# Kernel tuning notes

Hardware: AMD Instinct MI355X
Metric: run time of the kernel (lower is better)

Reference implementation:

```python
import jax, jax.numpy as jnp
import numpy as np

NEG_BIG = -9e15
ALPHA = 0.2  # leakyrelu slope


def setup_inputs() -> dict:
    key = jax.random.key(0)
    k1, k2, k3, k4 = jax.random.split(key, 4)
    N, Fin, Fout = 8192, 256, 256
    input = jax.random.normal(k1, (N, Fin), dtype=jnp.float32)
    adj = jax.random.randint(k2, (N, N), 0, 2, dtype=jnp.int32)
    W = jax.random.normal(k3, (Fin, Fout), dtype=jnp.float32) * (1.0 / np.sqrt(Fin))
    a = jax.random.normal(k4, (2 * Fout, 1), dtype=jnp.float32) * (1.0 / np.sqrt(Fout))
    return {"input": input, "adj": adj, "W": W, "a": a}


def reference(input, adj, W, a):
    # h: [N, F]
    h = input @ W
    Fout = h.shape[1]
    # Fused score: e_ij = leakyrelu(h_i . a[:F] + h_j . a[F:])
    s1 = h @ a[:Fout, 0]   # [N]
    s2 = h @ a[Fout:, 0]   # [N]
    e = s1[:, None] + s2[None, :]            # [N, N]
    e = jnp.where(e >= 0, e, ALPHA * e)      # leaky relu
    e = jnp.where(adj > 0, e, NEG_BIG)       # mask
    attention = jax.nn.softmax(e, axis=1)    # row softmax
    h_prime = attention @ h                  # [N, F]
    return jax.nn.elu(h_prime)               # concat=True -> elu
```

## Files before the change

### kernel.cpp

```cpp
#include <hip/hip_runtime.h>
#include <hip/hip_bf16.h>

#define LRALPHA 0.2f
#define LOG2E 1.4426950408889634f

typedef __attribute__((ext_vector_type(8))) short frag_ab;
typedef __attribute__((ext_vector_type(4))) float frag_cd;
typedef int   iv4 __attribute__((ext_vector_type(4)));
typedef float fv4 __attribute__((ext_vector_type(4)));
typedef float fv2 __attribute__((ext_vector_type(2)));
typedef unsigned int uv4 __attribute__((ext_vector_type(4)));

static __device__ __forceinline__ unsigned short f2bf(float f) {
  __hip_bfloat16 b = __float2bfloat16(f);
  unsigned short u;
  __builtin_memcpy(&u, &b, 2);
  return u;
}

static __device__ __forceinline__ uv4 make_w(const iv4* ca, const fv4* cv,
                                             float c1, float c2, float& zloc) {
  uv4 out;
#pragma unroll
  for (int g = 0; g < 2; ++g) {
#pragma unroll
    for (int h = 0; h < 2; ++h) {
      unsigned b0, b1;
#pragma unroll
      for (int e = 0; e < 2; ++e) {
        const int idx = h * 2 + e;
        const float u = fmaf(cv[g][idx], LOG2E, c1);
        const float m = fmaxf(u, LRALPHA * u);
        float w = exp2f(m - c2);
        w = ca[g][idx] ? w : 0.f;
        const unsigned bb = __float_as_uint(w);
        zloc += __uint_as_float(bb & 0xFFFF0000u);
        if (e == 0) b0 = bb; else b1 = bb;
      }
      out[g * 2 + h] = __builtin_amdgcn_perm(b1, b0, 0x07060302u);
    }
  }
  return out;
}

__global__ __launch_bounds__(256, 4) void gat_hproj(
    const float* __restrict__ X, const float* __restrict__ W,
    const float* __restrict__ avec,
    float* __restrict__ s1, float* __restrict__ s2,
    unsigned* __restrict__ s2key,
    unsigned short* __restrict__ hT) {
  const int tid = threadIdx.x;
  const int row0 = blockIdx.x * 16;
  const float* Xb = X + (size_t)row0 * 256;
  const int c = tid;

  fv2 acc2[8];
#pragma unroll
  for (int p = 0; p < 8; ++p) acc2[p] = (fv2){0.f, 0.f};

  for (int k = 0; k < 256; k += 4) {
    float wq[4];
#pragma unroll
    for (int i = 0; i < 4; ++i) wq[i] = W[(k + i) * 256 + c];
#pragma unroll
    for (int p = 0; p < 8; ++p) {
      const float* xr0 = Xb + (2 * p) * 256 + k;
      const float* xr1 = Xb + (2 * p + 1) * 256 + k;
#pragma unroll
      for (int i = 0; i < 4; ++i) {
        const fv2 xv = {xr0[i], xr1[i]};
        const fv2 wv = {wq[i], wq[i]};
        acc2[p] += xv * wv;
      }
    }
  }

  alignas(16) unsigned short hu[16];
#pragma unroll
  for (int r = 0; r < 16; ++r) hu[r] = f2bf(acc2[r >> 1][r & 1]);
  uv4* hdst = (uv4*)(hT + (size_t)c * 8192 + row0);
  hdst[0] = *(const uv4*)&hu[0];
  hdst[1] = *(const uv4*)&hu[8];

  const float a1c = avec[c];
  const float a2c = avec[256 + c];
  const int lane = tid & 63, wave = tid >> 6;
  __shared__ float r1[4][16], r2[4][16];
#pragma unroll
  for (int r = 0; r < 16; ++r) {
    const float av = acc2[r >> 1][r & 1];
    float v1 = av * a1c;
    float v2 = av * a2c;
#pragma unroll
    for (int off = 32; off > 0; off >>= 1) {
      v1 += __shfl_down(v1, off);
      v2 += __shfl_down(v2, off);
    }
    if (lane == 0) { r1[wave][r] = v1; r2[wave][r] = v2; }
  }
  __syncthreads();
  if (tid < 16) {
    const float v1 = r1[0][tid] + r1[1][tid] + r1[2][tid] + r1[3][tid];
    const float v2 = r2[0][tid] + r2[1][tid] + r2[2][tid] + r2[3][tid];
    s1[row0 + tid] = v1;
    s2[row0 + tid] = v2;
    float m = v2;
#pragma unroll
    for (int off = 8; off > 0; off >>= 1) m = fmaxf(m, __shfl_down(m, off));
    if (tid == 0) {
      const unsigned bits = __float_as_uint(m);
      const unsigned key = bits ^ ((unsigned)((int)bits >> 31) | 0x80000000u);
      atomicMax(s2key, key);
    }
  }
}

__global__ __launch_bounds__(512, 4) void gat_attn(
    const int* __restrict__ adj, const unsigned short* __restrict__ hT,
    const float* __restrict__ s1, const float* __restrict__ s2,
    const unsigned* __restrict__ s2keyp,
    float* __restrict__ pacc, float* __restrict__ pZ) {
  const int bid = blockIdx.x;
  const int x = bid & 7;
  const int ks = x >> 1;
  const int rb = ((bid >> 3) << 1) | (x & 1);
  const int row0 = rb * 64;
  const int jlo = ks * 2048;
  const int tid = threadIdx.x;
  const int wave = tid >> 6, lane = tid & 63;
  const int ln16 = lane & 15, quad = lane >> 4;

  __shared__ __align__(16) unsigned short P[2][64][72];
  __shared__ float Zred[64][8];

  const int r = tid >> 3, cq = tid & 7;
  const float s1r = s1[row0 + r];
  const unsigned key = s2keyp[0];
  const unsigned mb = (key & 0x80000000u) ? (key ^ 0x80000000u) : ~key;
  const float s2m = __uint_as_float(mb);
  const float tmv = s1r + s2m;
  const float mr = fmaxf(tmv, LRALPHA * tmv);
  const float c1 = s1r * LOG2E;
  const float c2 = mr * LOG2E;

  const int* adjRow = adj + (size_t)(row0 + r) * 8192 + jlo + cq * 8;
  const float* s2p = s2 + jlo + cq * 8;

  frag_cd acc[4][2];
  const frag_cd fz = {0.f, 0.f, 0.f, 0.f};
#pragma unroll
  for (int mi = 0; mi < 4; ++mi)
#pragma unroll
    for (int ni = 0; ni < 2; ++ni) acc[mi][ni] = fz;

  float zloc = 0.f;
  const int NIT = 2048 / 64;

  {
    iv4 ca[2]; fv4 cv[2];
    ca[0] = __builtin_nontemporal_load((const iv4*)(adjRow));
    ca[1] = __builtin_nontemporal_load((const iv4*)(adjRow + 4));
    cv[0] = *(const fv4*)(s2p);
    cv[1] = *(const fv4*)(s2p + 4);
    *(uv4*)&P[0][r][cq * 8] = make_w(ca, cv, c1, c2, zloc);
  }
  iv4 a[2];
  a[0] = __builtin_nontemporal_load((const iv4*)(adjRow + 64));
  a[1] = __builtin_nontemporal_load((const iv4*)(adjRow + 68));
  __syncthreads();

  for (int jt = 0; jt < NIT; ++jt) {
    const int cur = jt & 1, nxt = cur ^ 1;
    const size_t jbase = (size_t)(jlo + jt * 64);

    frag_ab bf[2][2];
#pragma unroll
    for (int kk = 0; kk < 2; ++kk)
#pragma unroll
      for (int ni = 0; ni < 2; ++ni) {
        const int f = wave * 32 + ni * 16 + ln16;
        bf[kk][ni] = *(const frag_ab*)(hT + (size_t)f * 8192 + jbase + kk * 32 + quad * 8);
      }

    iv4 a2[2];
    if (jt + 2 < NIT) {
      const int o = (jt + 2) * 64;
      a2[0] = __builtin_nontemporal_load((const iv4*)(adjRow + o));
      a2[1] = __builtin_nontemporal_load((const iv4*)(adjRow + o + 4));
    }

    if (jt + 1 < NIT) {
      const int o = (jt + 1) * 64;
      fv4 cv[2];
      cv[0] = *(const fv4*)(s2p + o);
      cv[1] = *(const fv4*)(s2p + o + 4);
      *(uv4*)&P[nxt][r][cq * 8] = make_w(a, cv, c1, c2, zloc);
    }

#pragma unroll
    for (int kk = 0; kk < 2; ++kk) {
      frag_ab af[4];
#pragma unroll
      for (int mi = 0; mi < 4; ++mi)
        af[mi] = *(const frag_ab*)&P[cur][mi * 16 + ln16][kk * 32 + quad * 8];
#pragma unroll
      for (int mi = 0; mi < 4; ++mi)
#pragma unroll
        for (int ni = 0; ni < 2; ++ni)
          acc[mi][ni] = __builtin_amdgcn_mfma_f32_16x16x32_bf16(
              af[mi], bf[kk][ni], acc[mi][ni], 0, 0, 0);
    }
    __syncthreads();
    a[0] = a2[0]; a[1] = a2[1];
  }

  Zred[r][cq] = zloc;
  __syncthreads();
  if (tid < 64) {
    float z = 0.f;
#pragma unroll
    for (int q = 0; q < 8; ++q) z += Zred[tid][q];
    pZ[ks * 8192 + row0 + tid] = z;
  }

  float* paccb = pacc + ((size_t)ks * 8192 + row0) * 256;
#pragma unroll
  for (int mi = 0; mi < 4; ++mi) {
#pragma unroll
    for (int ni = 0; ni < 2; ++ni) {
      const int f = wave * 32 + ni * 16 + ln16;
#pragma unroll
      for (int reg = 0; reg < 4; ++reg) {
        const int grow = mi * 16 + quad * 4 + reg;
        __builtin_nontemporal_store(acc[mi][ni][reg], paccb + (size_t)grow * 256 + f);
      }
    }
  }
}

__global__ __launch_bounds__(256) void gat_combine(
    const float* __restrict__ pacc, const float* __restrict__ pZ,
    float* __restrict__ out) {
  const int idx = blockIdx.x * 256 + threadIdx.x;
  const int row = idx >> 6;
  const float z = pZ[row] + pZ[8192 + row] + pZ[16384 + row] + pZ[24576 + row];
  const float invz = 1.f / z;
  const size_t PSTRIDE = (size_t)8192 * 256;
  const fv4 n0 = *(const fv4*)(pacc + (size_t)idx * 4);
  const fv4 n1 = *(const fv4*)(pacc + PSTRIDE + (size_t)idx * 4);
  const fv4 n2 = *(const fv4*)(pacc + 2 * PSTRIDE + (size_t)idx * 4);
  const fv4 n3 = *(const fv4*)(pacc + 3 * PSTRIDE + (size_t)idx * 4);
  fv4 o;
#pragma unroll
  for (int e = 0; e < 4; ++e) {
    const float vsum = (n0[e] + n1[e]) + (n2[e] + n3[e]);
    const float vv = vsum * invz;
    o[e] = vv > 0.f ? vv : expm1f(vv);
  }
  *(fv4*)(out + (size_t)idx * 4) = o;
}

extern "C" void kernel_launch(void* const* d_in, const int* in_sizes, int n_in,
                              void* d_out, int out_size, void* d_ws, size_t ws_size,
                              hipStream_t stream) {
  const float* X = (const float*)d_in[0];
  const int* adj = (const int*)d_in[1];
  const float* W = (const float*)d_in[2];
  const float* avec = (const float*)d_in[3];
  float* out = (float*)d_out;

  float* wsf = (float*)d_ws;
  float* s1 = wsf;
  float* s2 = wsf + 8192;
  unsigned* s2key = (unsigned*)(wsf + 16384);
  float* pZ = wsf + 24576;
  float* pacc = wsf + 65536;
  unsigned short* hT = (unsigned short*)(wsf + 65536 + 4 * 8192 * 256);

  hipLaunchKernelGGL(gat_hproj, dim3(512), dim3(256), 0, stream, X, W, avec, s1, s2, s2key, hT);
  hipLaunchKernelGGL(gat_attn, dim3(512), dim3(512), 0, stream, adj, hT, s1, s2, s2key, pacc, pZ);
  hipLaunchKernelGGL(gat_combine, dim3(2048), dim3(256), 0, stream, pacc, pZ, out);
}
```

Baseline: 489.4 us.

## Use 128-row tiles with 8-way column split and triple-buffered P tile

```diff
diff --git a/kernel.cpp b/kernel.cpp
--- a/kernel.cpp
+++ b/kernel.cpp
@@ -121,19 +121,18 @@
     const unsigned* __restrict__ s2keyp,
     float* __restrict__ pacc, float* __restrict__ pZ) {
   const int bid = blockIdx.x;
-  const int x = bid & 7;
-  const int ks = x >> 1;
-  const int rb = ((bid >> 3) << 1) | (x & 1);
-  const int row0 = rb * 64;
-  const int jlo = ks * 2048;
+  const int ks = bid & 7;
+  const int rg = bid >> 3;
+  const int row0 = rg * 128;
+  const int jlo = ks * 1024;
   const int tid = threadIdx.x;
   const int wave = tid >> 6, lane = tid & 63;
   const int ln16 = lane & 15, quad = lane >> 4;
 
-  __shared__ __align__(16) unsigned short P[2][64][72];
-  __shared__ float Zred[64][8];
-
-  const int r = tid >> 3, cq = tid & 7;
+  __shared__ __align__(16) unsigned short P[3][128][72];
+  __shared__ float Zred[128][4];
+
+  const int r = tid >> 2, cq = tid & 3;
   const float s1r = s1[row0 + r];
   const unsigned key = s2keyp[0];
   const unsigned mb = (key & 0x80000000u) ? (key ^ 0x80000000u) : ~key;
@@ -143,96 +142,74 @@
   const float c1 = s1r * LOG2E;
   const float c2 = mr * LOG2E;
 
-  const int* adjRow = adj + (size_t)(row0 + r) * 8192 + jlo + cq * 8;
-  const float* s2p = s2 + jlo + cq * 8;
-
-  frag_cd acc[4][2];
+  const int* adjRow = adj + (size_t)(row0 + r) * 8192 + jlo + cq * 16;
+  const float* s2p = s2 + jlo + cq * 16;
+
+  frag_cd acc[8][2];
   const frag_cd fz = {0.f, 0.f, 0.f, 0.f};
 #pragma unroll
-  for (int mi = 0; mi < 4; ++mi)
+  for (int mi = 0; mi < 8; ++mi)
 #pragma unroll
     for (int ni = 0; ni < 2; ++ni) acc[mi][ni] = fz;
 
   float zloc = 0.f;
-  const int NIT = 2048 / 64;
-
-  {
-    iv4 ca[2]; fv4 cv[2];
-    ca[0] = __builtin_nontemporal_load((const iv4*)(adjRow));
-    ca[1] = __builtin_nontemporal_load((const iv4*)(adjRow + 4));
-    cv[0] = *(const fv4*)(s2p);
-    cv[1] = *(const fv4*)(s2p + 4);
-    *(uv4*)&P[0][r][cq * 8] = make_w(ca, cv, c1, c2, zloc);
-  }
-  iv4 a[2];
-  a[0] = __builtin_nontemporal_load((const iv4*)(adjRow + 64));
-  a[1] = __builtin_nontemporal_load((const iv4*)(adjRow + 68));
-  __syncthreads();
-
+  const int NIT = 1024 / 64;
+
+  int cur = 0;
   for (int jt = 0; jt < NIT; ++jt) {
-    const int cur = jt & 1, nxt = cur ^ 1;
-    const size_t jbase = (size_t)(jlo + jt * 64);
-
-    frag_ab bf[2][2];
-#pragma unroll
-    for (int kk = 0; kk < 2; ++kk)
+    const int o = jt * 64;
+    iv4 ca[4]; fv4 cv[4];
+#pragma unroll
+    for (int q = 0; q < 4; ++q) {
+      ca[q] = __builtin_nontemporal_load((const iv4*)(adjRow + o + q * 4));
+      cv[q] = *(const fv4*)(s2p + o + q * 4);
+    }
+    const uv4 w0 = make_w(ca, cv, c1, c2, zloc);
+    const uv4 w1 = make_w(ca + 2, cv + 2, c1, c2, zloc);
+    *(uv4*)&P[cur][r][cq * 16] = w0;
+    *(uv4*)&P[cur][r][cq * 16 + 8] = w1;
+    __syncthreads();
+
+    const size_t jbase = (size_t)(jlo + o);
+#pragma unroll
+    for (int kk = 0; kk < 2; ++kk) {
+      frag_ab bf[2];
 #pragma unroll
       for (int ni = 0; ni < 2; ++ni) {
         const int f = wave * 32 + ni * 16 + ln16;
-        bf[kk][ni] = *(const frag_ab*)(hT + (size_t)f * 8192 + jbase + kk * 32 + quad * 8);
-      }
-
-    iv4 a2[2];
-    if (jt + 2 < NIT) {
-      const int o = (jt + 2) * 64;
-      a2[0] = __builtin_nontemporal_load((const iv4*)(adjRow + o));
-      a2[1] = __builtin_nontemporal_load((const iv4*)(adjRow + o + 4));
-    }
-
-    if (jt + 1 < NIT) {
-      const int o = (jt + 1) * 64;
-      fv4 cv[2];
-      cv[0] = *(const fv4*)(s2p + o);
-      cv[1] = *(const fv4*)(s2p + o + 4);
-      *(uv4*)&P[nxt][r][cq * 8] = make_w(a, cv, c1, c2, zloc);
-    }
-
-#pragma unroll
-    for (int kk = 0; kk < 2; ++kk) {
-      frag_ab af[4];
-#pragma unroll
-      for (int mi = 0; mi < 4; ++mi)
+        bf[ni] = *(const frag_ab*)(hT + (size_t)f * 8192 + jbase + kk * 32 + quad * 8);
+      }
+      frag_ab af[8];
+#pragma unroll
+      for (int mi = 0; mi < 8; ++mi)
         af[mi] = *(const frag_ab*)&P[cur][mi * 16 + ln16][kk * 32 + quad * 8];
 #pragma unroll
-      for (int mi = 0; mi < 4; ++mi)
+      for (int mi = 0; mi < 8; ++mi)
 #pragma unroll
         for (int ni = 0; ni < 2; ++ni)
           acc[mi][ni] = __builtin_amdgcn_mfma_f32_16x16x32_bf16(
-              af[mi], bf[kk][ni], acc[mi][ni], 0, 0, 0);
-    }
-    __syncthreads();
-    a[0] = a2[0]; a[1] = a2[1];
+              af[mi], bf[ni], acc[mi][ni], 0, 0, 0);
+    }
+    cur = cur + 1; if (cur == 3) cur = 0;
   }
 
   Zred[r][cq] = zloc;
   __syncthreads();
-  if (tid < 64) {
-    float z = 0.f;
-#pragma unroll
-    for (int q = 0; q < 8; ++q) z += Zred[tid][q];
-    pZ[ks * 8192 + row0 + tid] = z;
+  if (tid < 128) {
+    pZ[ks * 8192 + row0 + tid] =
+        Zred[tid][0] + Zred[tid][1] + Zred[tid][2] + Zred[tid][3];
   }
 
   float* paccb = pacc + ((size_t)ks * 8192 + row0) * 256;
 #pragma unroll
-  for (int mi = 0; mi < 4; ++mi) {
+  for (int mi = 0; mi < 8; ++mi) {
 #pragma unroll
     for (int ni = 0; ni < 2; ++ni) {
       const int f = wave * 32 + ni * 16 + ln16;
 #pragma unroll
       for (int reg = 0; reg < 4; ++reg) {
         const int grow = mi * 16 + quad * 4 + reg;
-        __builtin_nontemporal_store(acc[mi][ni][reg], paccb + (size_t)grow * 256 + f);
+        paccb[(size_t)grow * 256 + f] = acc[mi][ni][reg];
       }
     }
   }
@@ -243,18 +220,19 @@
     float* __restrict__ out) {
   const int idx = blockIdx.x * 256 + threadIdx.x;
   const int row = idx >> 6;
-  const float z = pZ[row] + pZ[8192 + row] + pZ[16384 + row] + pZ[24576 + row];
+  float z = 0.f;
+#pragma unroll
+  for (int s = 0; s < 8; ++s) z += pZ[s * 8192 + row];
   const float invz = 1.f / z;
   const size_t PSTRIDE = (size_t)8192 * 256;
-  const fv4 n0 = *(const fv4*)(pacc + (size_t)idx * 4);
-  const fv4 n1 = *(const fv4*)(pacc + PSTRIDE + (size_t)idx * 4);
-  const fv4 n2 = *(const fv4*)(pacc + 2 * PSTRIDE + (size_t)idx * 4);
-  const fv4 n3 = *(const fv4*)(pacc + 3 * PSTRIDE + (size_t)idx * 4);
+  fv4 vsum = {0.f, 0.f, 0.f, 0.f};
+#pragma unroll
+  for (int s = 0; s < 8; ++s)
+    vsum += *(const fv4*)(pacc + s * PSTRIDE + (size_t)idx * 4);
   fv4 o;
 #pragma unroll
   for (int e = 0; e < 4; ++e) {
-    const float vsum = (n0[e] + n1[e]) + (n2[e] + n3[e]);
-    const float vv = vsum * invz;
+    const float vv = vsum[e] * invz;
     o[e] = vv > 0.f ? vv : expm1f(vv);
   }
   *(fv4*)(out + (size_t)idx * 4) = o;
@@ -274,8 +252,8 @@
   float* s2 = wsf + 8192;
   unsigned* s2key = (unsigned*)(wsf + 16384);
   float* pZ = wsf + 24576;
-  float* pacc = wsf + 65536;
-  unsigned short* hT = (unsigned short*)(wsf + 65536 + 4 * 8192 * 256);
+  float* pacc = wsf + 131072;
+  unsigned short* hT = (unsigned short*)(wsf + 131072 + (size_t)8 * 8192 * 256);
 
   hipLaunchKernelGGL(gat_hproj, dim3(512), dim3(256), 0, stream, X, W, avec, s1, s2, s2key, hT);
   hipLaunchKernelGGL(gat_attn, dim3(512), dim3(512), 0, stream, adj, hT, s1, s2, s2key, pacc, pZ);
```

Measured after the change: 512.1 us. +4.6%, slower.
